# Kernel tuning notes

Hardware: AMD Instinct MI355X
Metric: run time of the kernel (lower is better)

Reference implementation:

```python
import jax, jax.numpy as jnp
import numpy as np

THRESHOLD = 1.0  # LIF firing threshold (single-step LIF: spike = heaviside(v - thr))


def _lif_spike(v):
    # single-step LIF: membrane = input, spike where membrane exceeds threshold
    return (v > THRESHOLD).astype(v.dtype)


def setup_inputs() -> dict:
    key = jax.random.key(0)
    ks = jax.random.split(key, 9)
    B, T, C = 2, 2048, 1024
    s = 1.0 / np.sqrt(C)
    return {
        "x": jax.random.normal(ks[0], (B, T, C), dtype=jnp.float32),
        "Wq": jax.random.normal(ks[1], (C, C), dtype=jnp.float32) * s,
        "bq": jnp.zeros((C,), dtype=jnp.float32),
        "Wk": jax.random.normal(ks[2], (C, C), dtype=jnp.float32) * s,
        "bk": jnp.zeros((C,), dtype=jnp.float32),
        "Wv": jax.random.normal(ks[3], (C, C), dtype=jnp.float32) * s,
        "bv": jnp.zeros((C,), dtype=jnp.float32),
        "Wo": jax.random.normal(ks[4], (C, C), dtype=jnp.float32) * s,
        "bo": jnp.zeros((C,), dtype=jnp.float32),
    }


def reference(x, Wq, bq, Wk, bk, Wv, bv, Wo, bo):
    B, T, C = x.shape
    H = 16
    D = C // H
    q = x @ Wq.T + bq
    k = x @ Wk.T + bk
    v = x @ Wv.T + bv
    # LIF spiking on q and k (binary spikes)
    qs = _lif_spike(q).reshape(B, T, H, D).transpose(0, 2, 1, 3)  # [B,H,T,D]
    ks = _lif_spike(k).reshape(B, T, H, D).transpose(0, 2, 1, 3)  # [B,H,T,D]
    vh = v.reshape(B, T, H, D).transpose(0, 2, 1, 3)              # [B,H,T,D]
    scores = jnp.einsum('bhqd,bhkd->bhqk', qs, ks) / jnp.sqrt(jnp.asarray(D, x.dtype))
    attn = jax.nn.softmax(scores, axis=-1)
    out = jnp.einsum('bhqk,bhkd->bhqd', attn, vh)                 # [B,H,T,D]
    out = out.transpose(0, 2, 1, 3).reshape(B, T, C)
    return out @ Wo.T + bo
```

## Files before the change

kernel.cpp:

```cpp
#include <hip/hip_runtime.h>
#include <cstdint>

typedef unsigned long long u64;
typedef unsigned int u32;
typedef unsigned short u16;
typedef __attribute__((ext_vector_type(8))) u16 u16x8;
typedef __attribute__((ext_vector_type(4))) u16 u16x4;
typedef __attribute__((ext_vector_type(8))) _Float16 f16x8;
typedef __attribute__((ext_vector_type(4))) float f32x4;

#define T_LEN 2048
#define C_DIM 1024
#define H_NUM 16
#define M_ROWS 4096
#define MB (1024ull * 1024ull)
#define TAU 3e-3f
#define FCAP 65536u
#define BLK_FCAP 512u

__device__ __forceinline__ u16 f2bf(float f) {
  unsigned u = __builtin_bit_cast(unsigned, f);
  return (u16)((u + 0x7FFFu + ((u >> 16) & 1u)) >> 16);
}
__device__ __forceinline__ u16 f2h(float f) {
  _Float16 h = (_Float16)f;
  return __builtin_bit_cast(u16, h);
}

__device__ __forceinline__ void async16(u16* lds, const u16* g) {
  __builtin_amdgcn_global_load_lds(
      (const __attribute__((address_space(1))) void*)g,
      (__attribute__((address_space(3))) void*)lds, 16, 0, 0);
}

__global__ __launch_bounds__(256) void split_all(
    const float* __restrict__ x,  const float* __restrict__ Wq,
    const float* __restrict__ Wk, const float* __restrict__ Wv,
    const float* __restrict__ Wo,
    u16* xh, u16* wq16, u16* wk16, u16* wv16, u16* woh, u32* flagcnt)
{
  const int i = blockIdx.x * 256 + threadIdx.x;
  if (i == 0) *flagcnt = 0;
  const float* src; u16* dst; int off; int isbf = 0;
  if      (i < 1048576) { src = x;  dst = xh;   off = i; }
  else if (i < 1310720) { src = Wq; dst = wq16; off = i - 1048576; }
  else if (i < 1572864) { src = Wk; dst = wk16; off = i - 1310720; }
  else if (i < 1835008) { src = Wv; dst = wv16; off = i - 1572864; }
  else                  { src = Wo; dst = woh;  off = i - 1835008; isbf = 1; }
  const float4 v = ((const float4*)src)[off];
  u16x4 h;
  if (isbf) {
    h[0] = f2bf(v.x); h[1] = f2bf(v.y); h[2] = f2bf(v.z); h[3] = f2bf(v.w);
  } else {
    h[0] = f2h(v.x);  h[1] = f2h(v.y);  h[2] = f2h(v.z);  h[3] = f2h(v.w);
  }
  ((u16x4*)dst)[off] = h;
}

__global__ __launch_bounds__(256) void mfma_qkv(
    const u16* __restrict__ A16,
    const u16* __restrict__ Bq16, const u16* __restrict__ Bk16,
    const u16* __restrict__ Bv16,
    const float* __restrict__ bq, const float* __restrict__ bk,
    const float* __restrict__ bv,
    u32* __restrict__ pbits, u32* __restrict__ flagcnt,
    u32* __restrict__ flaglist, u16* __restrict__ vT)
{
  __shared__ u16 Ahs[2][128][32];
  __shared__ u16 Bhs[2][64][32];
  __shared__ u32 fls[2 + BLK_FCAP];

  const int tid  = threadIdx.x;
  const int lane = tid & 63;
  const int w    = tid >> 6;
  const int wr   = w & 1;
  const int wc   = w >> 1;
  const int bm   = blockIdx.x * 128;
  const int bng  = blockIdx.y * 64;
  const int sel  = bng >> 10;
  const int bnl  = bng & 1023;

  const u16* Bh = (sel == 0) ? Bq16 : (sel == 1) ? Bk16 : Bv16;
  const float* bias = (sel == 0) ? bq : (sel == 1) ? bk : bv;

  if (tid == 0) fls[0] = 0;

  f32x4 acc[4][2];
  #pragma unroll
  for (int mf = 0; mf < 4; ++mf)
    #pragma unroll
    for (int nf = 0; nf < 2; ++nf) acc[mf][nf] = (f32x4){0.f, 0.f, 0.f, 0.f};

  const int sr = lane >> 2;
  const int sc = lane & 3;

#define STG(DST, SRC, TB, R0, KT)                                          \
  async16(&DST[(R0)][0],                                                   \
          &SRC[(size_t)((TB) + (R0) + sr) * 1024 + (KT) +                  \
               ((sc ^ ((((R0) + sr) >> 1) & 3)) << 3)]);

#define STAGE(B_, KT)                        \
  {                                          \
    STG(Ahs[B_], A16, bm, w * 32, KT);       \
    STG(Ahs[B_], A16, bm, w * 32 + 16, KT);  \
    STG(Bhs[B_], Bh, bnl, w * 16, KT);       \
  }

  STAGE(0, 0);
  __syncthreads();

  const int fr = lane & 15;
  const int fg = lane >> 4;
  int cur = 0;

  for (int kt = 0; kt < 1024; kt += 32) {
    if (kt + 32 < 1024) STAGE(cur ^ 1, kt + 32);

    f16x8 a_h[4], b_h[2];
    #pragma unroll
    for (int mf = 0; mf < 4; ++mf) {
      const int row = wr * 64 + mf * 16 + fr;
      const int cs = (fg ^ ((row >> 1) & 3)) << 3;
      a_h[mf] = __builtin_bit_cast(f16x8, *(const u16x8*)&Ahs[cur][row][cs]);
    }
    #pragma unroll
    for (int nf = 0; nf < 2; ++nf) {
      const int col = wc * 32 + nf * 16 + fr;
      const int cs = (fg ^ ((col >> 1) & 3)) << 3;
      b_h[nf] = __builtin_bit_cast(f16x8, *(const u16x8*)&Bhs[cur][col][cs]);
    }
    #pragma unroll
    for (int mf = 0; mf < 4; ++mf)
      #pragma unroll
      for (int nf = 0; nf < 2; ++nf)
        acc[mf][nf] = __builtin_amdgcn_mfma_f32_16x16x32_f16(a_h[mf], b_h[nf], acc[mf][nf], 0, 0, 0);
    __syncthreads();
    cur ^= 1;
  }
#undef STAGE
#undef STG

  if (sel < 2) {
    const int c0 = bnl + wc * 32 + fr;
    const int c1 = c0 + 16;
    const float bb0 = bias[c0];
    const float bb1 = bias[c1];
    const int head = bnl >> 6;
    #pragma unroll
    for (int mf = 0; mf < 4; ++mf) {
      const int row0 = bm + wr * 64 + mf * 16;
      #pragma unroll
      for (int j = 0; j < 4; ++j) {
        const float v0 = acc[mf][0][j] + bb0;
        const float v1 = acc[mf][1][j] + bb1;
        const u64 b0 = __ballot(v0 > 1.0f);
        const u64 b1 = __ballot(v1 > 1.0f);
        const int m = row0 + fg * 4 + j;
        if (fr == 0) {
          const u32 mask = (u32)((b0 >> (fg * 16)) & 0xFFFFu)
                         | ((u32)((b1 >> (fg * 16)) & 0xFFFFu) << 16);
          pbits[(((size_t)sel * 4096 + m) * 16 + head) * 2 + wc] = mask;
        }
        if (__builtin_fabsf(v0 - 1.0f) < TAU) {
          const u32 s = atomicAdd(&fls[0], 1u);
          if (s < BLK_FCAP) fls[2 + s] = ((u32)sel << 22) | ((u32)m << 10) | (u32)c0;
        }
        if (__builtin_fabsf(v1 - 1.0f) < TAU) {
          const u32 s = atomicAdd(&fls[0], 1u);
          if (s < BLK_FCAP) fls[2 + s] = ((u32)sel << 22) | ((u32)m << 10) | (u32)c1;
        }
      }
    }
    __syncthreads();
    const u32 cnt = fls[0] < BLK_FCAP ? fls[0] : BLK_FCAP;
    if (tid == 0) fls[1] = atomicAdd(flagcnt, cnt);
    __syncthreads();
    const u32 base = fls[1];
    for (u32 i = tid; i < cnt; i += 256) {
      const u32 pos = base + i;
      if (pos < FCAP) flaglist[pos] = fls[2 + i];
    }
  } else {
    #pragma unroll
    for (int mf = 0; mf < 4; ++mf) {
      const int row0 = bm + wr * 64 + mf * 16 + fg * 4;
      #pragma unroll
      for (int nf = 0; nf < 2; ++nf) {
        const int col = bnl + wc * 32 + nf * 16 + fr;
        const float bb = bias[col];
        const int bb_ = row0 >> 11, t0 = row0 & 2047;
        const int hh = col >> 6, dd = col & 63;
        u16x4 o;
        o[0] = f2bf(acc[mf][nf][0] + bb);
        o[1] = f2bf(acc[mf][nf][1] + bb);
        o[2] = f2bf(acc[mf][nf][2] + bb);
        o[3] = f2bf(acc[mf][nf][3] + bb);
        *(u16x4*)&vT[(((size_t)(bb_ * 16 + hh)) * 64 + dd) * 2048 + t0] = o;
      }
    }
  }
}

__global__ __launch_bounds__(256) void fix_bits(
    const float* __restrict__ x,
    const float* __restrict__ Wq, const float* __restrict__ Wk,
    const float* __restrict__ bq, const float* __restrict__ bk,
    u32* __restrict__ pbits,
    const u32* __restrict__ flagcnt, const u32* __restrict__ flaglist)
{
  u32 cnt = *flagcnt;
  if (cnt > FCAP) cnt = FCAP;
  const int lane = threadIdx.x & 63;
  const u32 wid  = (blockIdx.x * 256 + threadIdx.x) >> 6;
  const u32 nw   = gridDim.x * 4;
  for (u32 i = wid; i < cnt; i += nw) {
    const u32 e = flaglist[i];
    const int which = e >> 22;
    const int m = (e >> 10) & 4095;
    const int n = e & 1023;
    const float* W    = which ? Wk : Wq;
    const float* bias = which ? bk : bq;
    float s = 0.f;
    #pragma unroll
    for (int j = 0; j < 16; ++j)
      s += x[(size_t)m * 1024 + lane + j * 64] * W[(size_t)n * 1024 + lane + j * 64];
    #pragma unroll
    for (int off = 32; off > 0; off >>= 1) s += __shfl_xor(s, off);
    const float val = s + bias[n];
    if (lane == 0) {
      const size_t idx = (((size_t)which * 4096 + m) * 16 + (n >> 6)) * 2 + ((n >> 5) & 1);
      const u32 bit = 1u << (n & 31);
      const bool oldb = (pbits[idx] >> (n & 31)) & 1u;
      const bool newb = val > 1.0f;
      if (oldb != newb) atomicXor(&pbits[idx], bit);
    }
  }
}

__global__ __launch_bounds__(256) void attn_mfma(
    const u32* __restrict__ pbits, const u16* __restrict__ vT,
    u16* __restrict__ oh)
{
  __shared__ u16 vtb[64][72];
  __shared__ u64 kbt[68];
  __shared__ u32 wt_tab[65];

  const int tid = threadIdx.x, lane = tid & 63, w = tid >> 6;
  const int bid = ((blockIdx.x & 7) << 7) | (blockIdx.x >> 3);
  const int qt = bid & 31, bh = bid >> 5, b = bh >> 4, h = bh & 15;

  const int fr = lane & 15, fg = lane >> 4;

  if (tid < 65)
    wt_tab[tid] = __builtin_bit_cast(u32, exp2f((float)tid * 0.1803368801f));

  const int qm = b * T_LEN + qt * 64 + w * 16 + fr;
  const size_t qbase = (((size_t)qm) * 16 + h) * 2;
  const u32 qlo = pbits[qbase];
  const u32 qhi = pbits[qbase + 1];

  f32x4 acc[4];
  #pragma unroll
  for (int nf = 0; nf < 4; ++nf) acc[nf] = (f32x4){0.f, 0.f, 0.f, 0.f};
  f32x4 acc_z = (f32x4){0.f, 0.f, 0.f, 0.f};

  u16x8 ones;
  #pragma unroll
  for (int j = 0; j < 8; ++j) ones[j] = 0x3F80;

  const u16* vbase = vT + (size_t)bh * 64 * T_LEN;
  const int sd = tid >> 2, sk = (tid & 3) << 3;

  u16x8 r0, r1;
  u64 kbr = 0;
#define VLOAD(KT)                                                       \
  {                                                                     \
    r0 = *(const u16x8*)&vbase[(size_t)sd * T_LEN + (KT) + sk];         \
    r1 = *(const u16x8*)&vbase[(size_t)sd * T_LEN + (KT) + sk + 32];    \
  }
#define KLOAD(KT)                                                       \
  if (tid < 64) {                                                       \
    const int km = b * T_LEN + (KT) + tid;                              \
    const size_t kb = (((size_t)(4096 + km)) * 16 + h) * 2;             \
    kbr = (u64)pbits[kb] | ((u64)pbits[kb + 1] << 32);                  \
  }

  VLOAD(0);
  KLOAD(0);

  for (int kt = 0; kt < T_LEN; kt += 64) {
    *(u16x8*)&vtb[sd][sk]      = r0;
    *(u16x8*)&vtb[sd][sk + 32] = r1;
    if (tid < 64) kbt[tid + (tid >> 4)] = kbr;
    if (kt + 64 < T_LEN) { VLOAD(kt + 64); KLOAD(kt + 64); }
    __syncthreads();

    __builtin_amdgcn_s_setprio(1);
    #pragma unroll
    for (int ks = 0; ks < 2; ++ks) {
      u16x8 af;
      u32* afw = (u32*)&af;
      #pragma unroll
      for (int p = 0; p < 4; ++p) {
        const int kk = ks * 32 + fg * 8 + p * 2;
        const int pidx = kk + (kk >> 4);
        const u64 kb0 = kbt[pidx];
        const u64 kb1 = kbt[pidx + 1];
        const int mm0 = __builtin_popcount(qlo & (u32)kb0)
                      + __builtin_popcount(qhi & (u32)(kb0 >> 32));
        const int mm1 = __builtin_popcount(qlo & (u32)kb1)
                      + __builtin_popcount(qhi & (u32)(kb1 >> 32));
        const u32 t0 = wt_tab[mm0];
        const u32 t1 = wt_tab[mm1];
        afw[p] = (t1 & 0xFFFF0000u) | (t0 >> 16);
      }
      #pragma unroll
      for (int nf = 0; nf < 4; ++nf) {
        const u16x8 bfv = *(const u16x8*)&vtb[nf * 16 + fr][ks * 32 + fg * 8];
        acc[nf] = __builtin_amdgcn_mfma_f32_16x16x32_bf16(af, bfv, acc[nf], 0, 0, 0);
      }
      acc_z = __builtin_amdgcn_mfma_f32_16x16x32_bf16(af, ones, acc_z, 0, 0, 0);
    }
    __builtin_amdgcn_s_setprio(0);
    __syncthreads();
  }
#undef VLOAD
#undef KLOAD

  float invZ[4];
  #pragma unroll
  for (int j = 0; j < 4; ++j) invZ[j] = 1.0f / acc_z[j];

  #pragma unroll
  for (int nf = 0; nf < 4; ++nf) {
    const int col = h * 64 + nf * 16 + fr;
    #pragma unroll
    for (int j = 0; j < 4; ++j) {
      const int qrow = w * 16 + fg * 4 + j;
      const float o = acc[nf][j] * invZ[j];
      const size_t gq = (size_t)b * T_LEN + qt * 64 + qrow;
      oh[gq * 1024 + col] = f2bf(o);
    }
  }
}

__global__ __launch_bounds__(256) void mfma_out(
    const u16* __restrict__ Ah, const u16* __restrict__ Bh,
    const float* __restrict__ bias, float* __restrict__ out)
{
  __shared__ u16 Ahs[2][128][32];
  __shared__ u16 Bhs[2][64][32];

  const int tid  = threadIdx.x;
  const int lane = tid & 63;
  const int w    = tid >> 6;
  const int wr   = w & 1;
  const int wc   = w >> 1;
  const int bm   = blockIdx.x * 128;
  const int bn   = blockIdx.y * 64;

  f32x4 acc[4][2];
  #pragma unroll
  for (int mf = 0; mf < 4; ++mf)
    #pragma unroll
    for (int nf = 0; nf < 2; ++nf) acc[mf][nf] = (f32x4){0.f, 0.f, 0.f, 0.f};

  const int sr = lane >> 2;
  const int sc = lane & 3;

#define STG(DST, SRC, TB, R0, KT)                                          \
  async16(&DST[(R0)][0],                                                   \
          &SRC[(size_t)((TB) + (R0) + sr) * 1024 + (KT) +                  \
               ((sc ^ ((((R0) + sr) >> 1) & 3)) << 3)]);

#define STAGE(B_, KT)                        \
  {                                          \
    STG(Ahs[B_], Ah, bm, w * 32, KT);        \
    STG(Ahs[B_], Ah, bm, w * 32 + 16, KT);   \
    STG(Bhs[B_], Bh, bn, w * 16, KT);        \
  }

  STAGE(0, 0);
  __syncthreads();

  const int fr = lane & 15;
  const int fg = lane >> 4;
  int cur = 0;

  for (int kt = 0; kt < 1024; kt += 32) {
    if (kt + 32 < 1024) STAGE(cur ^ 1, kt + 32);

    u16x8 a_h[4], b_h[2];
    #pragma unroll
    for (int mf = 0; mf < 4; ++mf) {
      const int row = wr * 64 + mf * 16 + fr;
      const int cs = (fg ^ ((row >> 1) & 3)) << 3;
      a_h[mf] = *(const u16x8*)&Ahs[cur][row][cs];
    }
    #pragma unroll
    for (int nf = 0; nf < 2; ++nf) {
      const int col = wc * 32 + nf * 16 + fr;
      const int cs = (fg ^ ((col >> 1) & 3)) << 3;
      b_h[nf] = *(const u16x8*)&Bhs[cur][col][cs];
    }
    #pragma unroll
    for (int mf = 0; mf < 4; ++mf)
      #pragma unroll
      for (int nf = 0; nf < 2; ++nf)
        acc[mf][nf] = __builtin_amdgcn_mfma_f32_16x16x32_bf16(a_h[mf], b_h[nf], acc[mf][nf], 0, 0, 0);
    __syncthreads();
    cur ^= 1;
  }
#undef STAGE
#undef STG

  #pragma unroll
  for (int mf = 0; mf < 4; ++mf) {
    const int row0 = bm + wr * 64 + mf * 16 + fg * 4;
    #pragma unroll
    for (int nf = 0; nf < 2; ++nf) {
      const int col = bn + wc * 32 + nf * 16 + fr;
      const float bb = bias[col];
      #pragma unroll
      for (int j = 0; j < 4; ++j)
        out[(size_t)(row0 + j) * 1024 + col] = acc[mf][nf][j] + bb;
    }
  }
}

extern "C" void kernel_launch(void* const* d_in, const int* in_sizes, int n_in,
                              void* d_out, int out_size, void* d_ws, size_t ws_size,
                              hipStream_t stream) {
  const float* x  = (const float*)d_in[0];
  const float* Wq = (const float*)d_in[1];
  const float* bq = (const float*)d_in[2];
  const float* Wk = (const float*)d_in[3];
  const float* bk = (const float*)d_in[4];
  const float* Wv = (const float*)d_in[5];
  const float* bv = (const float*)d_in[6];
  const float* Wo = (const float*)d_in[7];
  const float* bo = (const float*)d_in[8];
  float* out = (float*)d_out;

  char* ws = (char*)d_ws;
  u16* oh   = (u16*)ws;
  u16* xh   = (u16*)(ws + 16 * MB);
  u16* vT   = (u16*)(ws + 32 * MB);
  u16* Woh  = (u16*)(ws + 40 * MB);
  u32* pbits = (u32*)(ws + 44 * MB);
  u32* flagcnt  = (u32*)(ws + 45 * MB);
  u32* flaglist = (u32*)(ws + 45 * MB + 256);

  char* dob = (char*)d_out;
  u16* Wq16 = (u16*)dob;
  u16* Wk16 = (u16*)(dob + 2 * MB);
  u16* Wv16 = (u16*)(dob + 4 * MB);

  split_all<<<8192, 256, 0, stream>>>(x, Wq, Wk, Wv, Wo,
                                      xh, Wq16, Wk16, Wv16, Woh, flagcnt);

  dim3 g1(M_ROWS / 128, 3072 / 64);
  mfma_qkv<<<g1, 256, 0, stream>>>(xh, Wq16, Wk16, Wv16,
                                   bq, bk, bv, pbits, flagcnt, flaglist, vT);

  fix_bits<<<256, 256, 0, stream>>>(x, Wq, Wk, bq, bk, pbits, flagcnt, flaglist);

  attn_mfma<<<32 * 32, 256, 0, stream>>>(pbits, vT, oh);

  dim3 g2(M_ROWS / 128, 1024 / 64);
  mfma_out<<<g2, 256, 0, stream>>>(oh, Woh, bo, out);
}
```

Before: 162.3 us.

## Compute Q, K and V projections in one block to reuse the staged A tile

Each QKV GEMM block now loads one 128x32 tile of x and multiplies it against the matching column tiles of Wq, Wk and Wv together, keeping three sets of accumulators. The grid shrinks from 48 to 16 column blocks. The aim is to cut the number of times x is loaded from global memory and written to LDS for the three projections to a third. In exchange, accumulator registers triple, LDS use grows, and there are fewer blocks (512 in place of 1536), which can lower occupancy and parallelism.

```diff
diff --git a/kernel.cpp b/kernel.cpp
--- a/kernel.cpp
+++ b/kernel.cpp
@@ -67,7 +67,9 @@
     u32* __restrict__ flaglist, u16* __restrict__ vT)
 {
   __shared__ u16 Ahs[2][128][32];
-  __shared__ u16 Bhs[2][64][32];
+  __shared__ u16 Bqs[2][64][32];
+  __shared__ u16 Bks[2][64][32];
+  __shared__ u16 Bvs[2][64][32];
   __shared__ u32 fls[2 + BLK_FCAP];
 
   const int tid  = threadIdx.x;
@@ -76,20 +78,17 @@
   const int wr   = w & 1;
   const int wc   = w >> 1;
   const int bm   = blockIdx.x * 128;
-  const int bng  = blockIdx.y * 64;
-  const int sel  = bng >> 10;
-  const int bnl  = bng & 1023;
-
-  const u16* Bh = (sel == 0) ? Bq16 : (sel == 1) ? Bk16 : Bv16;
-  const float* bias = (sel == 0) ? bq : (sel == 1) ? bk : bv;
+  const int bn   = blockIdx.y * 64;
 
   if (tid == 0) fls[0] = 0;
 
-  f32x4 acc[4][2];
-  #pragma unroll
-  for (int mf = 0; mf < 4; ++mf)
-    #pragma unroll
-    for (int nf = 0; nf < 2; ++nf) acc[mf][nf] = (f32x4){0.f, 0.f, 0.f, 0.f};
+  f32x4 acc[3][4][2];
+  #pragma unroll
+  for (int s = 0; s < 3; ++s)
+    #pragma unroll
+    for (int mf = 0; mf < 4; ++mf)
+      #pragma unroll
+      for (int nf = 0; nf < 2; ++nf) acc[s][mf][nf] = (f32x4){0.f, 0.f, 0.f, 0.f};
 
   const int sr = lane >> 2;
   const int sc = lane & 3;
@@ -103,7 +102,9 @@
   {                                          \
     STG(Ahs[B_], A16, bm, w * 32, KT);       \
     STG(Ahs[B_], A16, bm, w * 32 + 16, KT);  \
-    STG(Bhs[B_], Bh, bnl, w * 16, KT);       \
+    STG(Bqs[B_], Bq16, bn, w * 16, KT);      \
+    STG(Bks[B_], Bk16, bn, w * 16, KT);      \
+    STG(Bvs[B_], Bv16, bn, w * 16, KT);      \
   }
 
   STAGE(0, 0);
@@ -116,43 +117,66 @@
   for (int kt = 0; kt < 1024; kt += 32) {
     if (kt + 32 < 1024) STAGE(cur ^ 1, kt + 32);
 
-    f16x8 a_h[4], b_h[2];
+    f16x8 a_h[4];
     #pragma unroll
     for (int mf = 0; mf < 4; ++mf) {
       const int row = wr * 64 + mf * 16 + fr;
       const int cs = (fg ^ ((row >> 1) & 3)) << 3;
       a_h[mf] = __builtin_bit_cast(f16x8, *(const u16x8*)&Ahs[cur][row][cs]);
     }
-    #pragma unroll
-    for (int nf = 0; nf < 2; ++nf) {
-      const int col = wc * 32 + nf * 16 + fr;
-      const int cs = (fg ^ ((col >> 1) & 3)) << 3;
-      b_h[nf] = __builtin_bit_cast(f16x8, *(const u16x8*)&Bhs[cur][col][cs]);
-    }
-    #pragma unroll
-    for (int mf = 0; mf < 4; ++mf)
-      #pragma unroll
-      for (int nf = 0; nf < 2; ++nf)
-        acc[mf][nf] = __builtin_amdgcn_mfma_f32_16x16x32_f16(a_h[mf], b_h[nf], acc[mf][nf], 0, 0, 0);
+    const int col = wc * 32 + fr;
+    const int cs0 = (fg ^ (((wc * 32 + fr) >> 1) & 3)) << 3;
+    const int cs1 = (fg ^ (((wc * 32 + 16 + fr) >> 1) & 3)) << 3;
+    (void)col;
+
+    {
+      f16x8 b0 = __builtin_bit_cast(f16x8, *(const u16x8*)&Bqs[cur][wc * 32 + fr][cs0]);
+      f16x8 b1 = __builtin_bit_cast(f16x8, *(const u16x8*)&Bqs[cur][wc * 32 + 16 + fr][cs1]);
+      #pragma unroll
+      for (int mf = 0; mf < 4; ++mf) {
+        acc[0][mf][0] = __builtin_amdgcn_mfma_f32_16x16x32_f16(a_h[mf], b0, acc[0][mf][0], 0, 0, 0);
+        acc[0][mf][1] = __builtin_amdgcn_mfma_f32_16x16x32_f16(a_h[mf], b1, acc[0][mf][1], 0, 0, 0);
+      }
+    }
+    {
+      f16x8 b0 = __builtin_bit_cast(f16x8, *(const u16x8*)&Bks[cur][wc * 32 + fr][cs0]);
+      f16x8 b1 = __builtin_bit_cast(f16x8, *(const u16x8*)&Bks[cur][wc * 32 + 16 + fr][cs1]);
+      #pragma unroll
+      for (int mf = 0; mf < 4; ++mf) {
+        acc[1][mf][0] = __builtin_amdgcn_mfma_f32_16x16x32_f16(a_h[mf], b0, acc[1][mf][0], 0, 0, 0);
+        acc[1][mf][1] = __builtin_amdgcn_mfma_f32_16x16x32_f16(a_h[mf], b1, acc[1][mf][1], 0, 0, 0);
+      }
+    }
+    {
+      f16x8 b0 = __builtin_bit_cast(f16x8, *(const u16x8*)&Bvs[cur][wc * 32 + fr][cs0]);
+      f16x8 b1 = __builtin_bit_cast(f16x8, *(const u16x8*)&Bvs[cur][wc * 32 + 16 + fr][cs1]);
+      #pragma unroll
+      for (int mf = 0; mf < 4; ++mf) {
+        acc[2][mf][0] = __builtin_amdgcn_mfma_f32_16x16x32_f16(a_h[mf], b0, acc[2][mf][0], 0, 0, 0);
+        acc[2][mf][1] = __builtin_amdgcn_mfma_f32_16x16x32_f16(a_h[mf], b1, acc[2][mf][1], 0, 0, 0);
+      }
+    }
     __syncthreads();
     cur ^= 1;
   }
 #undef STAGE
 #undef STG
 
-  if (sel < 2) {
-    const int c0 = bnl + wc * 32 + fr;
+  const int head = bn >> 6;
+  #pragma unroll
+  for (int sel = 0; sel < 2; ++sel) {
+    const float* bias = sel ? bk : bq;
+    const int c0 = bn + wc * 32 + fr;
     const int c1 = c0 + 16;
     const float bb0 = bias[c0];
     const float bb1 = bias[c1];
-    const int head = bnl >> 6;
     #pragma unroll
     for (int mf = 0; mf < 4; ++mf) {
       const int row0 = bm + wr * 64 + mf * 16;
       #pragma unroll
       for (int j = 0; j < 4; ++j) {
-        const float v0 = acc[mf][0][j] + bb0;
-        const float v1 = acc[mf][1][j] + bb1;
+        const float v0 = acc[sel][mf][0][j] + bb0;
+        const float v1 = acc[sel][mf][1][j] + bb1;
         const u64 b0 = __ballot(v0 > 1.0f);
         const u64 b1 = __ballot(v1 > 1.0f);
         const int m = row0 + fg * 4 + j;
@@ -171,7 +195,9 @@
         }
       }
     }
-    __syncthreads();
+  }
+  __syncthreads();
+  {
     const u32 cnt = fls[0] < BLK_FCAP ? fls[0] : BLK_FCAP;
     if (tid == 0) fls[1] = atomicAdd(flagcnt, cnt);
     __syncthreads();
@@ -180,23 +206,23 @@
       const u32 pos = base + i;
       if (pos < FCAP) flaglist[pos] = fls[2 + i];
     }
-  } else {
-    #pragma unroll
-    for (int mf = 0; mf < 4; ++mf) {
-      const int row0 = bm + wr * 64 + mf * 16 + fg * 4;
-      #pragma unroll
-      for (int nf = 0; nf < 2; ++nf) {
-        const int col = bnl + wc * 32 + nf * 16 + fr;
-        const float bb = bias[col];
-        const int bb_ = row0 >> 11, t0 = row0 & 2047;
-        const int hh = col >> 6, dd = col & 63;
-        u16x4 o;
-        o[0] = f2bf(acc[mf][nf][0] + bb);
-        o[1] = f2bf(acc[mf][nf][1] + bb);
-        o[2] = f2bf(acc[mf][nf][2] + bb);
-        o[3] = f2bf(acc[mf][nf][3] + bb);
-        *(u16x4*)&vT[(((size_t)(bb_ * 16 + hh)) * 64 + dd) * 2048 + t0] = o;
-      }
+  }
+
+  #pragma unroll
+  for (int mf = 0; mf < 4; ++mf) {
+    const int row0 = bm + wr * 64 + mf * 16 + fg * 4;
+    #pragma unroll
+    for (int nf = 0; nf < 2; ++nf) {
+      const int col = bn + wc * 32 + nf * 16 + fr;
+      const float bbv = bv[col];
+      const int bb_ = row0 >> 11, t0 = row0 & 2047;
+      const int hh = col >> 6, dd = col & 63;
+      u16x4 o;
+      o[0] = f2bf(acc[2][mf][nf][0] + bbv);
+      o[1] = f2bf(acc[2][mf][nf][1] + bbv);
+      o[2] = f2bf(acc[2][mf][nf][2] + bbv);
+      o[3] = f2bf(acc[2][mf][nf][3] + bbv);
+      *(u16x4*)&vT[(((size_t)(bb_ * 16 + hh)) * 64 + dd) * 2048 + t0] = o;
     }
   }
 }
@@ -459,7 +485,7 @@
   split_all<<<8192, 256, 0, stream>>>(x, Wq, Wk, Wv, Wo,
                                       xh, Wq16, Wk16, Wv16, Woh, flagcnt);
 
-  dim3 g1(M_ROWS / 128, 3072 / 64);
+  dim3 g1(M_ROWS / 128, 1024 / 64);
   mfma_qkv<<<g1, 256, 0, stream>>>(xh, Wq16, Wk16, Wv16,
                                    bq, bk, bv, pbits, flagcnt, flaglist, vT);
 
```

After: 145.4 us. 10.4% less time.
